# Performance work log

Hardware: AMD Instinct MI355X
Metric: run time of the kernel (lower is better)

The kernel has to match this reference:

```python
import jax, jax.numpy as jnp
import numpy as np

LN_EPS = 1e-5

def _liquid_layer(x, A, B, C, K, ab, g, bt):
    # x: [batch, T, in_dim]; precompute input projections once.
    uB = jnp.einsum('bti,is->bts', x, B)                                  # [B, T, S]
    uB_prev = jnp.concatenate([jnp.zeros_like(uB[:, :1]), uB[:, :-1]], axis=1)

    def step(h, xs):
        u, up = xs                                                        # each [B, S]
        z = h @ A + ab + u + (h @ K) * up                                 # liquid interaction
        mu = jnp.mean(z, axis=-1, keepdims=True)
        var = jnp.mean(jnp.square(z - mu), axis=-1, keepdims=True)
        zn = (z - mu) * jax.lax.rsqrt(var + LN_EPS) * g + bt
        h = h + jax.nn.gelu(zn, approximate=False)                        # torch GELU is exact
        return h, h

    h0 = jnp.zeros((x.shape[0], A.shape[0]), x.dtype)
    _, hs = jax.lax.scan(step, h0, (jnp.swapaxes(uB, 0, 1), jnp.swapaxes(uB_prev, 0, 1)))
    hs = jnp.swapaxes(hs, 0, 1)                                           # [B, T, S]
    return jnp.einsum('bts,so->bto', hs, C)


def setup_inputs() -> dict:
    key = jax.random.key(0)
    ks = jax.random.split(key, 9)
    B, T, D = 16, 2048, 512
    S = 512
    scale = 1.0 / np.sqrt(S)  # xavier-like scale
    inp = {
        'x':  jax.random.normal(ks[0], (B, T, D), jnp.float32),
        'A0': jax.random.normal(ks[1], (S, S), jnp.float32) * scale,
        'B0': jax.random.normal(ks[2], (D, S), jnp.float32) * scale,
        'C0': jax.random.normal(ks[3], (S, S), jnp.float32) * scale,
        'K0': jax.random.normal(ks[4], (S, S), jnp.float32) * scale,
        'ab0': jnp.zeros((S,), jnp.float32),
        'g0':  jnp.ones((S,), jnp.float32),
        'bt0': jnp.zeros((S,), jnp.float32),
        'A1': jax.random.normal(ks[5], (S, S), jnp.float32) * scale,
        'B1': jax.random.normal(ks[6], (S, S), jnp.float32) * scale,
        'C1': jax.random.normal(ks[7], (S, D), jnp.float32) * scale,
        'K1': jax.random.normal(ks[8], (S, S), jnp.float32) * scale,
        'ab1': jnp.zeros((S,), jnp.float32),
        'g1':  jnp.ones((S,), jnp.float32),
        'bt1': jnp.zeros((S,), jnp.float32),
    }
    return inp


def reference(x, A0, B0, C0, K0, ab0, g0, bt0, A1, B1, C1, K1, ab1, g1, bt1):
    y = _liquid_layer(x, A0, B0, C0, K0, ab0, g0, bt0)
    y = _liquid_layer(y, A1, B1, C1, K1, ab1, g1, bt1)
    return y
```

## Files before the change

### kernel.cpp

```cpp
#include <hip/hip_runtime.h>

using half8 = __attribute__((ext_vector_type(8))) _Float16;
using f32x4 = __attribute__((ext_vector_type(4))) float;
typedef unsigned long long u64;

static constexpr int TT  = 2048;
static constexpr int NB  = 16;
static constexpr int SS  = 512;
static constexpr int NWG = 8;
static constexpr int NT  = 2;
static constexpr int NBT = 8;
static constexpr int HSLOT = 8;

__global__ __launch_bounds__(256) void tcvt_kernel(const float* __restrict__ in,
                                                   _Float16* __restrict__ out) {
    __shared__ float tile[32][33];
    int bid = blockIdx.x;
    int rb = (bid >> 4) * 32, cb = (bid & 15) * 32;
    int tx = threadIdx.x & 31, ty = threadIdx.x >> 5;
    for (int rr = ty; rr < 32; rr += 8)
        tile[rr][tx] = in[(size_t)(rb + rr) * SS + cb + tx];
    __syncthreads();
    for (int rr = ty; rr < 32; rr += 8)
        out[(size_t)(cb + rr) * SS + rb + tx] = (_Float16)tile[tx][rr];
}

__global__ __launch_bounds__(256) void wpack_kernel(const float* __restrict__ in,
                                                    _Float16* __restrict__ out) {
    int idx = blockIdx.x * blockDim.x + threadIdx.x;
    int kk = idx >> 9, c = idx & 511;
    half8 v;
    #pragma unroll
    for (int j = 0; j < 8; ++j) v[j] = (_Float16)in[(size_t)(kk * 8 + j) * SS + c];
    *(half8*)(out + (size_t)idx * 8) = v;
}

__global__ __launch_bounds__(256) void wmm_kernel(const float* __restrict__ C0,
                                                  const float* __restrict__ B1,
                                                  float* __restrict__ W) {
    int k = blockIdx.x;
    int tid = threadIdx.x;
    const float* crow = C0 + (size_t)k * SS;
    float s0 = 0.f, s1 = 0.f;
    for (int m = 0; m < SS; ++m) {
        float cv = crow[m];
        s0 += cv * B1[(size_t)m * SS + tid];
        s1 += cv * B1[(size_t)m * SS + tid + 256];
    }
    W[(size_t)k * SS + tid] = s0;
    W[(size_t)k * SS + tid + 256] = s1;
}

__global__ __launch_bounds__(512) void zinit_kernel(unsigned* __restrict__ p, int n) {
    int i = blockIdx.x * blockDim.x + threadIdx.x;
    if (i < n) p[i] = 0u;
}

template <int ALAY, int MODE>
__global__ __launch_bounds__(256) void gemm_kernel(const void* __restrict__ Aptr,
                                                   const _Float16* __restrict__ BT,
                                                   void* __restrict__ Outp) {
    int lane = threadIdx.x & 63;
    int wv   = threadIdx.x >> 6;
    int wid  = blockIdx.x * 4 + wv;
    int mt   = wid >> 3;
    int nb   = (wid & 7) * 64;
    int mbase = mt * 16;
    int lo = lane & 15, q = lane >> 4;

    f32x4 acc[4] = {{0,0,0,0},{0,0,0,0},{0,0,0,0},{0,0,0,0}};

    const float*    Af = (const float*)Aptr;
    const _Float16* Ah = (const _Float16*)Aptr;
    size_t arow = (size_t)(mbase + lo) * SS;

    #pragma unroll 2
    for (int kk = 0; kk < 16; ++kk) {
        int koff = kk * 32 + q * 8;
        half8 af;
        if (ALAY == 0) {
            const float* ar = Af + arow + koff;
            f32x4 a0 = *(const f32x4*)ar;
            f32x4 a1 = *(const f32x4*)(ar + 4);
            #pragma unroll
            for (int j = 0; j < 4; ++j) { af[j] = (_Float16)a0[j]; af[4 + j] = (_Float16)a1[j]; }
        } else {
            af = *(const half8*)(Ah + arow + koff);
        }
        #pragma unroll
        for (int j = 0; j < 4; ++j) {
            int n = nb + j * 16 + lo;
            half8 bf = *(const half8*)(BT + (size_t)n * SS + koff);
            acc[j] = __builtin_amdgcn_mfma_f32_16x16x32_f16(af, bf, acc[j], 0, 0, 0);
        }
    }

    #pragma unroll
    for (int j = 0; j < 4; ++j) {
        #pragma unroll
        for (int i = 0; i < 4; ++i) {
            int m = mbase + q * 4 + i;
            int n = nb + j * 16 + lo;
            if (MODE == 0) {
                ((_Float16*)Outp)[(size_t)m * SS + n] = (_Float16)acc[j][i];
            } else if (MODE == 1) {
                ((float*)Outp)[(size_t)m * SS + n] = acc[j][i];
            } else {
                int t2 = m & (TT - 1);
                int b2 = m >> 11;
                ((_Float16*)Outp)[((size_t)t2 * NB + b2) * SS + n] = (_Float16)acc[j][i];
            }
        }
    }
}

__global__ __launch_bounds__(512) void scan15_kernel(
        const _Float16* __restrict__ U,
        const _Float16* __restrict__ PA0,
        const _Float16* __restrict__ PK0,
        const float* __restrict__ ab0, const float* __restrict__ gn0, const float* __restrict__ bt0,
        const _Float16* __restrict__ PA1,
        const _Float16* __restrict__ PK1,
        const _Float16* __restrict__ PW,
        const float* __restrict__ ab1, const float* __restrict__ gn1, const float* __restrict__ bt1,
        _Float16* __restrict__ hs1,
        u64*      __restrict__ zmail,
        u64*      __restrict__ smail,
        unsigned* __restrict__ flags,
        _Float16* __restrict__ hmail)
{
    const int layer = blockIdx.x >> 4;
    const int team  = (blockIdx.x >> 3) & 1;
    const int wg    = blockIdx.x & 7;
    const int btm   = team * NBT;
    const int tid   = threadIdx.x;
    const int wv    = tid >> 6;
    const int lane  = tid & 63;
    const int q     = lane >> 4;
    const int r     = lane & 15;

    const _Float16* PA  = layer ? PA1 : PA0;
    const _Float16* PK  = layer ? PK1 : PK0;
    const float*    abp = layer ? ab1 : ab0;
    const float*    gnp = layer ? gn1 : gn0;
    const float*    btp = layer ? bt1 : bt0;

    const int pg = layer * 2 + team;
    u64*      zmailT = zmail + (size_t)pg * (2 * NWG * 256);
    u64*      smailT = smail + (size_t)pg * (2 * NWG * 8);
    unsigned* flagsT = flags + (size_t)pg * (NWG * 32);
    unsigned* flagsO = flags + (size_t)((1 - layer) * 2 + team) * (NWG * 32);
    _Float16* hmailT = hmail + (size_t)team * (HSLOT * NBT * SS);

    __shared__ _Float16 H16[16][520];
    __shared__ _Float16 H0[16][520];
    alignas(16) __shared__ float ZW32[8][64];
    __shared__ float STAT[4][16][2];
    __shared__ float GG[512], BB[512];

    const int ub = tid & 7;
    const int ug = tid >> 3;
    const int uc = ug * 8;
    const int ow = ug >> 3;

    for (int e = tid; e < 16 * 520; e += 512) {
        (&H16[0][0])[e] = (_Float16)0.f;
        (&H0[0][0])[e]  = (_Float16)0.f;
    }
    GG[tid] = gnp[tid];
    BB[tid] = btp[tid];

    const bool mf = (wv < 4);
    const int ccol = wg * 64 + (wv & 3) * 16 + r;
    const float abreg = abp[ccol];

    float hreg[8];
    #pragma unroll
    for (int i = 0; i < 8; ++i) hreg[i] = 0.f;
    float uprev[4] = {0.f, 0.f, 0.f, 0.f};
    float ucur[4]  = {0.f, 0.f, 0.f, 0.f};
    if (layer == 0 && mf && q < 2) {
        #pragma unroll
        for (int i = 0; i < 4; ++i)
            ucur[i] = (float)U[(size_t)(btm + q * 4 + i) * SS + ccol];
    }
    __syncthreads();

    if (layer == 1) {
        if (wv == 0 && lane < 8) {
            while (__hip_atomic_load(&flagsO[lane * 32], __ATOMIC_RELAXED,
                                     __HIP_MEMORY_SCOPE_AGENT) < 2u) {}
        }
        __syncthreads();
        {
            const u64* hp = (const u64*)(hmailT + ((size_t)0 * NBT + ub) * SS + uc);
            union { u64 u[2]; half8 h; } hv;
            hv.u[0] = __hip_atomic_load(hp + 0, __ATOMIC_RELAXED, __HIP_MEMORY_SCOPE_AGENT);
            hv.u[1] = __hip_atomic_load(hp + 1, __ATOMIC_RELAXED, __HIP_MEMORY_SCOPE_AGENT);
            *(half8*)&H0[ub][uc] = hv.h;
        }
        __syncthreads();
    }

    for (int t = 0; t < TT; ++t) {
        const int par = t & 1;

        if (mf) {
            f32x4 zA = {0.f, 0.f, 0.f, 0.f}, zK = {0.f, 0.f, 0.f, 0.f};
            #pragma unroll
            for (int ks = 0; ks < 16; ++ks) {
                half8 hf = *(const half8*)(&H16[r][ks * 32 + q * 8]);
                half8 wa = *(const half8*)(PA + (((size_t)(ks * 4 + q)) * SS + ccol) * 8);
                half8 wk = *(const half8*)(PK + (((size_t)(ks * 4 + q)) * SS + ccol) * 8);
                zA = __builtin_amdgcn_mfma_f32_16x16x32_f16(hf, wa, zA, 0, 0, 0);
                zK = __builtin_amdgcn_mfma_f32_16x16x32_f16(hf, wk, zK, 0, 0, 0);
            }
            if (layer == 1) {
                f32x4 ua = {0.f, 0.f, 0.f, 0.f};
                #pragma unroll
                for (int ks = 0; ks < 16; ++ks) {
                    half8 h0f = *(const half8*)(&H0[r][ks * 32 + q * 8]);
                    half8 ww  = *(const half8*)(PW + (((size_t)(ks * 4 + q)) * SS + ccol) * 8);
                    ua = __builtin_amdgcn_mfma_f32_16x16x32_f16(h0f, ww, ua, 0, 0, 0);
                }
                #pragma unroll
                for (int i = 0; i < 4; ++i) ucur[i] = ua[i];
            }

            float z[4];
            #pragma unroll
            for (int i = 0; i < 4; ++i) {
                z[i] = zA[i] + ucur[i] + abreg + zK[i] * uprev[i];
                uprev[i] = ucur[i];
            }
            if (q < 2) {
                #pragma unroll
                for (int i = 0; i < 4; ++i)
                    ZW32[q * 4 + i][(wv & 3) * 16 + r] = z[i];
            }

            float s1[4], s2[4];
            #pragma unroll
            for (int i = 0; i < 4; ++i) { s1[i] = z[i]; s2[i] = z[i] * z[i]; }
            #pragma unroll
            for (int off = 1; off < 16; off <<= 1) {
                #pragma unroll
                for (int i = 0; i < 4; ++i) {
                    s1[i] += __shfl_xor(s1[i], off, 64);
                    s2[i] += __shfl_xor(s2[i], off, 64);
                }
            }
            if (r == 0) {
                #pragma unroll
                for (int i = 0; i < 4; ++i) {
                    STAT[wv][q * 4 + i][0] = s1[i];
                    STAT[wv][q * 4 + i][1] = s2[i];
                }
            }
        }
        __syncthreads();

        if (tid < 256) {
            u64 v = ((const u64*)ZW32)[tid];
            __hip_atomic_store(&zmailT[((size_t)par * NWG + wg) * 256 + tid], v,
                               __ATOMIC_RELAXED, __HIP_MEMORY_SCOPE_AGENT);
        }
        if (wv == 0 && lane < NBT) {
            float S1 = STAT[0][lane][0] + STAT[1][lane][0] + STAT[2][lane][0] + STAT[3][lane][0];
            float S2 = STAT[0][lane][1] + STAT[1][lane][1] + STAT[2][lane][1] + STAT[3][lane][1];
            union { float f[2]; u64 u; } pk;
            pk.f[0] = S1; pk.f[1] = S2;
            __hip_atomic_store(&smailT[((size_t)par * NWG + wg) * 8 + lane], pk.u,
                               __ATOMIC_RELAXED, __HIP_MEMORY_SCOPE_AGENT);
        }
        if (layer == 0 && mf && q < 2) {
            const int tn = (t + 1 < TT) ? (t + 1) : t;
            #pragma unroll
            for (int i = 0; i < 4; ++i)
                ucur[i] = (float)U[((size_t)tn * NB + btm + q * 4 + i) * SS + ccol];
        }
        __builtin_amdgcn_s_waitcnt(0);
        __syncthreads();

        if (tid == 0)
            __hip_atomic_store(&flagsT[wg * 32], (unsigned)(t + 1),
                               __ATOMIC_RELAXED, __HIP_MEMORY_SCOPE_AGENT);
        if (wv == 0 && lane >= 1 && lane < NWG) {
            unsigned* fp = &flagsT[((wg + lane) & (NWG - 1)) * 32];
            while (__hip_atomic_load(fp, __ATOMIC_RELAXED, __HIP_MEMORY_SCOPE_AGENT)
                   < (unsigned)(t + 1)) {}
        }
        if (wv == 0 && lane >= 8 && lane < 16) {
            unsigned thr;
            if (layer == 0) thr = (t > 7) ? (unsigned)(t - 7) : 0u;
            else            thr = (t + 1 < TT) ? (unsigned)(t + 3) : 0u;
            if (thr) {
                unsigned* fp = &flagsO[(lane - 8) * 32];
                while (__hip_atomic_load(fp, __ATOMIC_RELAXED, __HIP_MEMORY_SCOPE_AGENT) < thr) {}
            }
        }
        __syncthreads();

        float zz[8];
        if (ow == wg) {
            #pragma unroll
            for (int i = 0; i < 8; ++i) zz[i] = ZW32[ub][(uc & 63) + i];
        } else {
            union { u64 u[4]; float f[8]; } zu;
            const u64* src = &zmailT[((size_t)par * NWG + ow) * 256 + ub * 32 + ((uc & 63) >> 1)];
            #pragma unroll
            for (int i = 0; i < 4; ++i)
                zu.u[i] = __hip_atomic_load(src + i, __ATOMIC_RELAXED, __HIP_MEMORY_SCOPE_AGENT);
            #pragma unroll
            for (int i = 0; i < 8; ++i) zz[i] = zu.f[i];
        }
        float S1 = 0.f, S2 = 0.f;
        #pragma unroll
        for (int i = 0; i < NWG; ++i) {
            union { u64 u; float f[2]; } pk;
            pk.u = __hip_atomic_load(&smailT[((size_t)par * NWG + i) * 8 + ub],
                                     __ATOMIC_RELAXED, __HIP_MEMORY_SCOPE_AGENT);
            S1 += pk.f[0]; S2 += pk.f[1];
        }
        const float mu  = S1 * (1.0f / SS);
        const float var = S2 * (1.0f / SS) - mu * mu;
        const float rs  = rsqrtf(var + 1e-5f);

        half8 hh;
        #pragma unroll
        for (int i4 = 0; i4 < 2; ++i4) {
            f32x4 gq = *(const f32x4*)&GG[uc + i4 * 4];
            f32x4 bq = *(const f32x4*)&BB[uc + i4 * 4];
            #pragma unroll
            for (int jj = 0; jj < 4; ++jj) {
                const int e = i4 * 4 + jj;
                float zn = (zz[e] - mu) * rs * gq[jj] + bq[jj];
                float ge = 0.5f * zn * (1.0f + erff(zn * 0.70710678118654752f));
                hreg[e] += ge;
                hh[e] = (_Float16)hreg[e];
            }
        }
        *(half8*)(&H16[ub][uc]) = hh;

        if (layer == 0) {
            if (ow == wg) {
                u64* hp = (u64*)(hmailT + (((size_t)(t & (HSLOT - 1))) * NBT + ub) * SS + uc);
                union { half8 h; u64 u[2]; } hv; hv.h = hh;
                __hip_atomic_store(hp + 0, hv.u[0], __ATOMIC_RELAXED, __HIP_MEMORY_SCOPE_AGENT);
                __hip_atomic_store(hp + 1, hv.u[1], __ATOMIC_RELAXED, __HIP_MEMORY_SCOPE_AGENT);
            }
        } else {
            if (ow == wg)
                *(half8*)(hs1 + ((size_t)(btm + ub) * TT + t) * SS + uc) = hh;
            if (t + 1 < TT) {
                const u64* hp = (const u64*)(hmailT
                                + (((size_t)((t + 1) & (HSLOT - 1))) * NBT + ub) * SS + uc);
                union { u64 u[2]; half8 h; } hv;
                hv.u[0] = __hip_atomic_load(hp + 0, __ATOMIC_RELAXED, __HIP_MEMORY_SCOPE_AGENT);
                hv.u[1] = __hip_atomic_load(hp + 1, __ATOMIC_RELAXED, __HIP_MEMORY_SCOPE_AGENT);
                *(half8*)&H0[ub][uc] = hv.h;
            }
        }
        __syncthreads();
    }

    if (layer == 0) {
        __builtin_amdgcn_s_waitcnt(0);
        __syncthreads();
        if (tid == 0)
            __hip_atomic_store(&flagsT[wg * 32], (unsigned)(TT + 1),
                               __ATOMIC_RELAXED, __HIP_MEMORY_SCOPE_AGENT);
    }
}

extern "C" void kernel_launch(void* const* d_in, const int* in_sizes, int n_in,
                              void* d_out, int out_size, void* d_ws, size_t ws_size,
                              hipStream_t stream) {
    const float* x   = (const float*)d_in[0];
    const float* A0  = (const float*)d_in[1];
    const float* B0  = (const float*)d_in[2];
    const float* C0  = (const float*)d_in[3];
    const float* K0  = (const float*)d_in[4];
    const float* ab0 = (const float*)d_in[5];
    const float* g0  = (const float*)d_in[6];
    const float* bt0 = (const float*)d_in[7];
    const float* A1  = (const float*)d_in[8];
    const float* B1  = (const float*)d_in[9];
    const float* C1  = (const float*)d_in[10];
    const float* K1  = (const float*)d_in[11];
    const float* ab1 = (const float*)d_in[12];
    const float* g1  = (const float*)d_in[13];
    const float* bt1 = (const float*)d_in[14];

    char* ws = (char*)d_ws;
    size_t off = 0;
    auto alloc = [&](size_t bytes) { size_t o = off; off = (off + bytes + 255) & ~(size_t)255; return o; };

    const size_t BUF_BYTES = (size_t)NB * TT * SS * 2;
    const size_t WP_BYTES  = (size_t)SS * SS * 2;

    _Float16* U0  = (_Float16*)(ws + alloc(BUF_BYTES));
    _Float16* hs1 = (_Float16*)(ws + alloc(BUF_BYTES));
    _Float16* B0T = (_Float16*)(ws + alloc(WP_BYTES));
    _Float16* C1T = (_Float16*)(ws + alloc(WP_BYTES));
    _Float16* PA0 = (_Float16*)(ws + alloc(WP_BYTES));
    _Float16* PK0 = (_Float16*)(ws + alloc(WP_BYTES));
    _Float16* PA1 = (_Float16*)(ws + alloc(WP_BYTES));
    _Float16* PK1 = (_Float16*)(ws + alloc(WP_BYTES));
    _Float16* PW  = (_Float16*)(ws + alloc(WP_BYTES));
    float*    Wf  = (float*)(ws + alloc((size_t)SS * SS * 4));
    u64*      zmail = (u64*)(ws + alloc((size_t)4 * 2 * NWG * 256 * 8));
    u64*      smail = (u64*)(ws + alloc((size_t)4 * 2 * NWG * 8 * 8));
    unsigned* flags = (unsigned*)(ws + alloc((size_t)4 * NWG * 32 * 4));
    _Float16* hmail = (_Float16*)(ws + alloc((size_t)NT * HSLOT * NBT * SS * 2));

    zinit_kernel<<<2, 512, 0, stream>>>(flags, 4 * NWG * 32);

    tcvt_kernel<<<256, 256, 0, stream>>>(B0, B0T);
    tcvt_kernel<<<256, 256, 0, stream>>>(C1, C1T);
    wmm_kernel<<<512, 256, 0, stream>>>(C0, B1, Wf);
    wpack_kernel<<<128, 256, 0, stream>>>(A0, PA0);
    wpack_kernel<<<128, 256, 0, stream>>>(K0, PK0);
    wpack_kernel<<<128, 256, 0, stream>>>(A1, PA1);
    wpack_kernel<<<128, 256, 0, stream>>>(K1, PK1);
    wpack_kernel<<<128, 256, 0, stream>>>(Wf, PW);

    gemm_kernel<0, 2><<<4096, 256, 0, stream>>>((const void*)x, B0T, (void*)U0);

    scan15_kernel<<<32, 512, 0, stream>>>(U0, PA0, PK0, ab0, g0, bt0,
                                          PA1, PK1, PW, ab1, g1, bt1,
                                          hs1, zmail, smail, flags, hmail);

    gemm_kernel<1, 1><<<4096, 256, 0, stream>>>((const void*)hs1, C1T, d_out);
}
```

Baseline: 14.56 ms.

## Move layer-1 input projection into layer-0 blocks and mail fp32 results

The product of the layer-0 hidden state with the fused C0·B1 weight (PW) is now computed by the layer-0 workgroups right after each step. They publish the fp32 result through a ring mailbox, and layer-1 workgroups prefetch it for the next step. Layer 1 no longer receives fp16 hidden states or runs an extra 16-MFMA chain on its critical recurrent path, so that work is balanced onto the layer-0 producer. The trade-off is that layer 0's per-step critical path grows, and the mailbox now carries fp32 partial outputs whose ring-slot timing must stay correct.

```diff
diff --git a/kernel.cpp b/kernel.cpp
--- a/kernel.cpp
+++ b/kernel.cpp
@@ -11,6 +11,7 @@
 static constexpr int NT  = 2;
 static constexpr int NBT = 8;
 static constexpr int HSLOT = 8;
+static constexpr int U1SLOT = NWG * 4 * 2 * 16 * 2;
 
 __global__ __launch_bounds__(256) void tcvt_kernel(const float* __restrict__ in,
                                                    _Float16* __restrict__ out) {
@@ -114,7 +115,7 @@
     }
 }
 
-__global__ __launch_bounds__(512) void scan15_kernel(
+__global__ __launch_bounds__(512) void scan17_kernel(
         const _Float16* __restrict__ U,
         const _Float16* __restrict__ PA0,
         const _Float16* __restrict__ PK0,
@@ -127,7 +128,7 @@
         u64*      __restrict__ zmail,
         u64*      __restrict__ smail,
         unsigned* __restrict__ flags,
-        _Float16* __restrict__ hmail)
+        u64*      __restrict__ u1mail)
 {
     const int layer = blockIdx.x >> 4;
     const int team  = (blockIdx.x >> 3) & 1;
@@ -146,14 +147,13 @@
     const float*    btp = layer ? bt1 : bt0;
 
     const int pg = layer * 2 + team;
-    u64*      zmailT = zmail + (size_t)pg * (2 * NWG * 256);
-    u64*      smailT = smail + (size_t)pg * (2 * NWG * 8);
-    unsigned* flagsT = flags + (size_t)pg * (NWG * 32);
-    unsigned* flagsO = flags + (size_t)((1 - layer) * 2 + team) * (NWG * 32);
-    _Float16* hmailT = hmail + (size_t)team * (HSLOT * NBT * SS);
+    u64*      zmailT  = zmail + (size_t)pg * (2 * NWG * 256);
+    u64*      smailT  = smail + (size_t)pg * (2 * NWG * 8);
+    unsigned* flagsT  = flags + (size_t)pg * (NWG * 32);
+    unsigned* flagsO  = flags + (size_t)((1 - layer) * 2 + team) * (NWG * 32);
+    u64*      u1mailT = u1mail + (size_t)team * HSLOT * U1SLOT;
 
     __shared__ _Float16 H16[16][520];
-    __shared__ _Float16 H0[16][520];
     alignas(16) __shared__ float ZW32[8][64];
     __shared__ float STAT[4][16][2];
     __shared__ float GG[512], BB[512];
@@ -163,22 +163,25 @@
     const int uc = ug * 8;
     const int ow = ug >> 3;
 
-    for (int e = tid; e < 16 * 520; e += 512) {
-        (&H16[0][0])[e] = (_Float16)0.f;
-        (&H0[0][0])[e]  = (_Float16)0.f;
-    }
+    for (int e = tid; e < 16 * 520; e += 512) (&H16[0][0])[e] = (_Float16)0.f;
     GG[tid] = gnp[tid];
     BB[tid] = btp[tid];
 
     const bool mf = (wv < 4);
     const int ccol = wg * 64 + (wv & 3) * 16 + r;
     const float abreg = abp[ccol];
+
+    auto u1addr = [&](int slot) -> u64* {
+        return u1mailT + ((((size_t)slot * NWG + wg) * 4 + (wv & 3)) * 2 + q) * 32 + r * 2;
+    };
 
     float hreg[8];
     #pragma unroll
     for (int i = 0; i < 8; ++i) hreg[i] = 0.f;
     float uprev[4] = {0.f, 0.f, 0.f, 0.f};
     float ucur[4]  = {0.f, 0.f, 0.f, 0.f};
+    float unext[4] = {0.f, 0.f, 0.f, 0.f};
+    float uapub[4] = {0.f, 0.f, 0.f, 0.f};
     if (layer == 0 && mf && q < 2) {
         #pragma unroll
         for (int i = 0; i < 4; ++i)
@@ -192,20 +195,23 @@
                                      __HIP_MEMORY_SCOPE_AGENT) < 2u) {}
         }
         __syncthreads();
-        {
-            const u64* hp = (const u64*)(hmailT + ((size_t)0 * NBT + ub) * SS + uc);
-            union { u64 u[2]; half8 h; } hv;
-            hv.u[0] = __hip_atomic_load(hp + 0, __ATOMIC_RELAXED, __HIP_MEMORY_SCOPE_AGENT);
-            hv.u[1] = __hip_atomic_load(hp + 1, __ATOMIC_RELAXED, __HIP_MEMORY_SCOPE_AGENT);
-            *(half8*)&H0[ub][uc] = hv.h;
-        }
-        __syncthreads();
+        if (mf && q < 2) {
+            const u64* up = u1addr(0);
+            union { u64 u; float f[2]; } a, b;
+            a.u = __hip_atomic_load(up + 0, __ATOMIC_RELAXED, __HIP_MEMORY_SCOPE_AGENT);
+            b.u = __hip_atomic_load(up + 1, __ATOMIC_RELAXED, __HIP_MEMORY_SCOPE_AGENT);
+            unext[0] = a.f[0]; unext[1] = a.f[1]; unext[2] = b.f[0]; unext[3] = b.f[1];
+        }
     }
 
     for (int t = 0; t < TT; ++t) {
         const int par = t & 1;
 
         if (mf) {
+            if (layer == 1) {
+                #pragma unroll
+                for (int i = 0; i < 4; ++i) ucur[i] = unext[i];
+            }
             f32x4 zA = {0.f, 0.f, 0.f, 0.f}, zK = {0.f, 0.f, 0.f, 0.f};
             #pragma unroll
             for (int ks = 0; ks < 16; ++ks) {
@@ -215,16 +221,16 @@
                 zA = __builtin_amdgcn_mfma_f32_16x16x32_f16(hf, wa, zA, 0, 0, 0);
                 zK = __builtin_amdgcn_mfma_f32_16x16x32_f16(hf, wk, zK, 0, 0, 0);
             }
-            if (layer == 1) {
+            if (layer == 0) {
                 f32x4 ua = {0.f, 0.f, 0.f, 0.f};
                 #pragma unroll
                 for (int ks = 0; ks < 16; ++ks) {
-                    half8 h0f = *(const half8*)(&H0[r][ks * 32 + q * 8]);
-                    half8 ww  = *(const half8*)(PW + (((size_t)(ks * 4 + q)) * SS + ccol) * 8);
-                    ua = __builtin_amdgcn_mfma_f32_16x16x32_f16(h0f, ww, ua, 0, 0, 0);
+                    half8 hf = *(const half8*)(&H16[r][ks * 32 + q * 8]);
+                    half8 ww = *(const half8*)(PW + (((size_t)(ks * 4 + q)) * SS + ccol) * 8);
+                    ua = __builtin_amdgcn_mfma_f32_16x16x32_f16(hf, ww, ua, 0, 0, 0);
                 }
                 #pragma unroll
-                for (int i = 0; i < 4; ++i) ucur[i] = ua[i];
+                for (int i = 0; i < 4; ++i) uapub[i] = ua[i];
             }
 
             float z[4];
@@ -274,6 +280,12 @@
                                __ATOMIC_RELAXED, __HIP_MEMORY_SCOPE_AGENT);
         }
         if (layer == 0 && mf && q < 2) {
+            u64* up = u1addr((t - 1) & (HSLOT - 1));
+            union { float f[2]; u64 u; } p0, p1;
+            p0.f[0] = uapub[0]; p0.f[1] = uapub[1];
+            p1.f[0] = uapub[2]; p1.f[1] = uapub[3];
+            __hip_atomic_store(up + 0, p0.u, __ATOMIC_RELAXED, __HIP_MEMORY_SCOPE_AGENT);
+            __hip_atomic_store(up + 1, p1.u, __ATOMIC_RELAXED, __HIP_MEMORY_SCOPE_AGENT);
             const int tn = (t + 1 < TT) ? (t + 1) : t;
             #pragma unroll
             for (int i = 0; i < 4; ++i)
@@ -301,6 +313,14 @@
         }
         __syncthreads();
 
+        if (layer == 1 && mf && q < 2 && t + 1 < TT) {
+            const u64* up = u1addr((t + 1) & (HSLOT - 1));
+            union { u64 u; float f[2]; } a, b;
+            a.u = __hip_atomic_load(up + 0, __ATOMIC_RELAXED, __HIP_MEMORY_SCOPE_AGENT);
+            b.u = __hip_atomic_load(up + 1, __ATOMIC_RELAXED, __HIP_MEMORY_SCOPE_AGENT);
+            unext[0] = a.f[0]; unext[1] = a.f[1]; unext[2] = b.f[0]; unext[3] = b.f[1];
+        }
+
         float zz[8];
         if (ow == wg) {
             #pragma unroll
@@ -341,30 +361,29 @@
             }
         }
         *(half8*)(&H16[ub][uc]) = hh;
-
-        if (layer == 0) {
-            if (ow == wg) {
-                u64* hp = (u64*)(hmailT + (((size_t)(t & (HSLOT - 1))) * NBT + ub) * SS + uc);
-                union { half8 h; u64 u[2]; } hv; hv.h = hh;
-                __hip_atomic_store(hp + 0, hv.u[0], __ATOMIC_RELAXED, __HIP_MEMORY_SCOPE_AGENT);
-                __hip_atomic_store(hp + 1, hv.u[1], __ATOMIC_RELAXED, __HIP_MEMORY_SCOPE_AGENT);
-            }
-        } else {
-            if (ow == wg)
-                *(half8*)(hs1 + ((size_t)(btm + ub) * TT + t) * SS + uc) = hh;
-            if (t + 1 < TT) {
-                const u64* hp = (const u64*)(hmailT
-                                + (((size_t)((t + 1) & (HSLOT - 1))) * NBT + ub) * SS + uc);
-                union { u64 u[2]; half8 h; } hv;
-                hv.u[0] = __hip_atomic_load(hp + 0, __ATOMIC_RELAXED, __HIP_MEMORY_SCOPE_AGENT);
-                hv.u[1] = __hip_atomic_load(hp + 1, __ATOMIC_RELAXED, __HIP_MEMORY_SCOPE_AGENT);
-                *(half8*)&H0[ub][uc] = hv.h;
-            }
-        }
+        if (layer == 1 && ow == wg)
+            *(half8*)(hs1 + ((size_t)(btm + ub) * TT + t) * SS + uc) = hh;
         __syncthreads();
     }
 
     if (layer == 0) {
+        if (mf) {
+            f32x4 ua = {0.f, 0.f, 0.f, 0.f};
+            #pragma unroll
+            for (int ks = 0; ks < 16; ++ks) {
+                half8 hf = *(const half8*)(&H16[r][ks * 32 + q * 8]);
+                half8 ww = *(const half8*)(PW + (((size_t)(ks * 4 + q)) * SS + ccol) * 8);
+                ua = __builtin_amdgcn_mfma_f32_16x16x32_f16(hf, ww, ua, 0, 0, 0);
+            }
+            if (q < 2) {
+                u64* up = u1addr((TT - 1) & (HSLOT - 1));
+                union { float f[2]; u64 u; } p0, p1;
+                p0.f[0] = ua[0]; p0.f[1] = ua[1];
+                p1.f[0] = ua[2]; p1.f[1] = ua[3];
+                __hip_atomic_store(up + 0, p0.u, __ATOMIC_RELAXED, __HIP_MEMORY_SCOPE_AGENT);
+                __hip_atomic_store(up + 1, p1.u, __ATOMIC_RELAXED, __HIP_MEMORY_SCOPE_AGENT);
+            }
+        }
         __builtin_amdgcn_s_waitcnt(0);
         __syncthreads();
         if (tid == 0)
@@ -409,10 +428,10 @@
     _Float16* PK1 = (_Float16*)(ws + alloc(WP_BYTES));
     _Float16* PW  = (_Float16*)(ws + alloc(WP_BYTES));
     float*    Wf  = (float*)(ws + alloc((size_t)SS * SS * 4));
-    u64*      zmail = (u64*)(ws + alloc((size_t)4 * 2 * NWG * 256 * 8));
-    u64*      smail = (u64*)(ws + alloc((size_t)4 * 2 * NWG * 8 * 8));
-    unsigned* flags = (unsigned*)(ws + alloc((size_t)4 * NWG * 32 * 4));
-    _Float16* hmail = (_Float16*)(ws + alloc((size_t)NT * HSLOT * NBT * SS * 2));
+    u64*      zmail  = (u64*)(ws + alloc((size_t)4 * 2 * NWG * 256 * 8));
+    u64*      smail  = (u64*)(ws + alloc((size_t)4 * 2 * NWG * 8 * 8));
+    unsigned* flags  = (unsigned*)(ws + alloc((size_t)4 * NWG * 32 * 4));
+    u64*      u1mail = (u64*)(ws + alloc((size_t)NT * HSLOT * U1SLOT * 8));
 
     zinit_kernel<<<2, 512, 0, stream>>>(flags, 4 * NWG * 32);
 
@@ -427,9 +446,9 @@
 
     gemm_kernel<0, 2><<<4096, 256, 0, stream>>>((const void*)x, B0T, (void*)U0);
 
-    scan15_kernel<<<32, 512, 0, stream>>>(U0, PA0, PK0, ab0, g0, bt0,
+    scan17_kernel<<<32, 512, 0, stream>>>(U0, PA0, PK0, ab0, g0, bt0,
                                           PA1, PK1, PW, ab1, g1, bt1,
-                                          hs1, zmail, smail, flags, hmail);
+                                          hs1, zmail, smail, flags, u1mail);
 
     gemm_kernel<1, 1><<<4096, 256, 0, stream>>>((const void*)hs1, C1T, d_out);
 }
```

Measured after the change: 13.98 ms. 4.0% less time.
